# Optimization experiments

Hardware: AMD Instinct MI355X
Metric: run time of the kernel (lower is better)

## Reference

```python
import jax, jax.numpy as jnp
import numpy as np

N = 20000      # nodes
E = 320000     # edges (before self loops)
C = 128        # hidesize (in = out channels)
H = 5          # attention heads
NEG_SLOPE = 0.2
EPS = 1e-16


def setup_inputs() -> dict:
    key = jax.random.key(0)
    k1, k2, k3, k4, k5, k6 = jax.random.split(key, 6)
    features = jax.random.normal(k1, (N, C), dtype=jnp.float32)
    edge_index = jax.random.randint(k2, (2, E), 0, N, dtype=jnp.int64)
    # GATConv parameters: shared linear for src/dst, per-head attention vectors, bias
    W = jax.random.normal(k3, (C, H * C), dtype=jnp.float32) * (1.0 / np.sqrt(C))
    att_src = jax.random.normal(k4, (H, C), dtype=jnp.float32) * 0.1
    att_dst = jax.random.normal(k5, (H, C), dtype=jnp.float32) * 0.1
    bias = jax.random.normal(k6, (C,), dtype=jnp.float32) * 0.1
    return {"features": features, "W": W, "att_src": att_src,
            "att_dst": att_dst, "bias": bias, "edge_index": edge_index}


def _gat_forward(features, W, att_src, att_dst, bias, edge_index):
    n = features.shape[0]
    # add_self_loops=True: append (i -> i) for every node
    loop = jnp.arange(n, dtype=edge_index.dtype)
    src = jnp.concatenate([edge_index[0], loop])  # message source j
    dst = jnp.concatenate([edge_index[1], loop])  # aggregation target i

    h = (features @ W).reshape(n, H, C)           # [N,H,C] projected per head
    alpha_src = jnp.sum(h * att_src, axis=-1)     # [N,H]
    alpha_dst = jnp.sum(h * att_dst, axis=-1)     # [N,H]

    e = alpha_src[src] + alpha_dst[dst]           # [E',H]
    e = jax.nn.leaky_relu(e, negative_slope=NEG_SLOPE)

    # segment softmax over edges grouped by destination node
    e_max = jax.ops.segment_max(e, dst, num_segments=n)   # [N,H]
    e = jnp.exp(e - e_max[dst])
    denom = jax.ops.segment_sum(e, dst, num_segments=n)   # [N,H]
    alpha = e / (denom[dst] + EPS)                         # [E',H]

    msg = h[src] * alpha[:, :, None]                       # [E',H,C]
    out = jax.ops.segment_sum(msg, dst, num_segments=n)    # [N,H,C]
    out = out.mean(axis=1) + bias                          # concat=False -> head mean
    return features + out                                  # use_residual=True


def reference(features, W, att_src, att_dst, bias, edge_index):
    return _gat_forward(features, W, att_src, att_dst, bias, edge_index)
```

## Files before the change

kernel.cpp:

```cpp
#include <hip/hip_runtime.h>
#include <hip/hip_bf16.h>
#include <stdint.h>

#define C_DIM 128
#define H_DIM 5
#define PAD_DEG 64

typedef __bf16 bf16x8 __attribute__((ext_vector_type(8)));
typedef float f32x4 __attribute__((ext_vector_type(4)));
typedef float f32x2 __attribute__((ext_vector_type(2)));

static __device__ __forceinline__ ushort f2bf(float x) {
    __hip_bfloat16 b = __float2bfloat16(x);
    return *reinterpret_cast<ushort*>(&b);
}

__global__ __launch_bounds__(256) void prep0_kernel(
    const float* __restrict__ F, const float* __restrict__ W,
    const float* __restrict__ att_src, const float* __restrict__ att_dst,
    ushort* __restrict__ Abf, ushort* __restrict__ Bt, float* __restrict__ Wa,
    const int* __restrict__ srcArr, const int* __restrict__ dstArr,
    int* __restrict__ cnt, int* __restrict__ colp,
    int Bw, int Bb, int Bc, int N, int E) {
    int b = blockIdx.x;
    int tid = threadIdx.x;
    if (b < Bw) {
        int t = b * 256 + tid;
        if (t < C_DIM * 10) {
            int k = t / 10, j = t % 10;
            int h = j % 5;
            const float* att = ((j < 5) ? att_src : att_dst) + h * C_DIM;
            const float* w = W + (size_t)k * (H_DIM * C_DIM) + h * C_DIM;
            float sum = 0.f;
#pragma unroll 8
            for (int c = 0; c < C_DIM; ++c) sum = fmaf(w[c], att[c], sum);
            Wa[k * 10 + j] = sum;
        }
    } else if (b < Bw + Bb) {
        int t = (b - Bw) * 256 + tid;
        if (t < 640 * 128) {
            int c = t >> 7, k = t & 127;
            Bt[t] = f2bf(W[(size_t)k * 640 + c]);
        }
    } else if (b < Bw + Bb + Bc) {
        int t = (b - Bw - Bb) * 256 + tid;
        if (t < N * 16) {
            const float4* f4 = reinterpret_cast<const float4*>(F) + (size_t)t * 2;
            float4 v0 = f4[0], v1 = f4[1];
            float vv[8] = {v0.x, v0.y, v0.z, v0.w, v1.x, v1.y, v1.z, v1.w};
            ushort u[8];
#pragma unroll
            for (int i = 0; i < 8; ++i) u[i] = f2bf(vv[i]);
            *reinterpret_cast<uint4*>(Abf + (size_t)t * 8) = *reinterpret_cast<uint4*>(u);
        }
    } else {
        int e = (b - Bw - Bb - Bc) * 256 + tid;
        if (e < E + N) {
            int s, i;
            if (e < E) { s = srcArr[e]; i = dstArr[e]; }
            else       { s = e - E;    i = s; }
            int pos = atomicAdd(&cnt[i], 1);
            if (pos < PAD_DEG) colp[(size_t)i * PAD_DEG + pos] = s;
        }
    }
}

__global__ __launch_bounds__(256) void gemm_alpha_kernel(
    const ushort* __restrict__ Abf, const ushort* __restrict__ Bt,
    unsigned char* __restrict__ Hout,
    const float* __restrict__ F, const float* __restrict__ Wa,
    float* __restrict__ asrc, float* __restrict__ adst,
    int NBG, int NRB, int N) {
    __shared__ char smem[52224];
    int tid = threadIdx.x;
    if ((int)blockIdx.x < NBG) {
        ushort (*As)[136] = reinterpret_cast<ushort(*)[136]>(smem);
        ushort (*Bs)[136] = reinterpret_cast<ushort(*)[136]>(smem + 128 * 136 * 2);
        int by = blockIdx.x % NRB;
        int bx = blockIdx.x / NRB;
        int row0 = by * 128, col0 = bx * 64;
        int seg = tid & 15, rb = tid >> 4;
#pragma unroll
        for (int p = 0; p < 8; ++p) {
            int r = rb + p * 16;
            int gr = row0 + r;
            uint4 v = make_uint4(0u, 0u, 0u, 0u);
            if (gr < N) v = *reinterpret_cast<const uint4*>(Abf + (size_t)gr * 128 + seg * 8);
            *reinterpret_cast<uint4*>(&As[r][seg * 8]) = v;
        }
#pragma unroll
        for (int p = 0; p < 4; ++p) {
            int r = rb + p * 16;
            uint4 v = *reinterpret_cast<const uint4*>(Bt + (size_t)(col0 + r) * 128 + seg * 8);
            *reinterpret_cast<uint4*>(&Bs[r][seg * 8]) = v;
        }
        __syncthreads();
        int wave = tid >> 6, lane = tid & 63;
        int wr = (wave & 1) * 64;
        int wc = (wave >> 1) * 32;
        int lm = lane & 15, lk = (lane >> 4) * 8;
        f32x4 acc[4][2] = {};
#pragma unroll
        for (int kk = 0; kk < 4; ++kk) {
            int k = kk * 32 + lk;
            bf16x8 a[4], bvec[2];
#pragma unroll
            for (int m = 0; m < 4; ++m)
                a[m] = *reinterpret_cast<const bf16x8*>(&As[wr + m * 16 + lm][k]);
#pragma unroll
            for (int n = 0; n < 2; ++n)
                bvec[n] = *reinterpret_cast<const bf16x8*>(&Bs[wc + n * 16 + lm][k]);
#pragma unroll
            for (int m = 0; m < 4; ++m)
#pragma unroll
                for (int n = 0; n < 2; ++n)
                    acc[m][n] = __builtin_amdgcn_mfma_f32_16x16x32_bf16(a[m], bvec[n], acc[m][n], 0, 0, 0);
        }
        int r4 = (lane >> 4) * 4;
#pragma unroll
        for (int m = 0; m < 4; ++m) {
#pragma unroll
            for (int r = 0; r < 4; ++r) {
                int grow = row0 + wr + m * 16 + r4 + r;
                if (grow < N) {
                    int pk = __builtin_amdgcn_cvt_pk_fp8_f32(acc[m][0][r], acc[m][1][r], 0, false);
                    unsigned char* rowp = Hout + (size_t)grow * 640 + col0 + wc;
                    rowp[lm]      = (unsigned char)(pk & 0xff);
                    rowp[16 + lm] = (unsigned char)((pk >> 8) & 0xff);
                }
            }
        }
    } else {
        float (*f_lds)[132] = reinterpret_cast<float(*)[132]>(smem);
        float* wa_lds = reinterpret_cast<float*>(smem + 16 * 132 * 4);
        int node0 = ((int)blockIdx.x - NBG) * 16;
#pragma unroll
        for (int t = 0; t < 2; ++t) {
            int idx = tid + t * 256;
            int n = idx >> 5, c4 = idx & 31;
            int node = node0 + n;
            float4 v = make_float4(0.f, 0.f, 0.f, 0.f);
            if (node < N) v = *(reinterpret_cast<const float4*>(F) + (size_t)node * 32 + c4);
            f_lds[n][c4 * 4 + 0] = v.x;
            f_lds[n][c4 * 4 + 1] = v.y;
            f_lds[n][c4 * 4 + 2] = v.z;
            f_lds[n][c4 * 4 + 3] = v.w;
        }
#pragma unroll
        for (int t = 0; t < 5; ++t) {
            int idx = tid + t * 256;
            if (idx < 1280) wa_lds[idx] = Wa[idx];
        }
        __syncthreads();
        if (tid < 160) {
            int n = tid / 10, j = tid % 10;
            int node = node0 + n;
            if (node < N) {
                float sum = 0.f;
#pragma unroll 8
                for (int k = 0; k < C_DIM; ++k) sum = fmaf(f_lds[n][k], wa_lds[k * 10 + j], sum);
                if (j < 5) asrc[node * 5 + j] = sum;
                else       adst[node * 5 + (j - 5)] = sum;
            }
        }
    }
}

__global__ __launch_bounds__(256) void gat_aggregate(
    const int* __restrict__ cnt, const int* __restrict__ colp,
    const float* __restrict__ asrc, const float* __restrict__ adst,
    const unsigned char* __restrict__ h8,
    const float* __restrict__ features, const float* __restrict__ bias,
    float* __restrict__ out, int N) {
    int node = blockIdx.x * 4 + (threadIdx.x >> 6);
    if (node >= N) return;
    int lane = threadIdx.x & 63;
    int g = lane >> 4, m = lane & 15;
    float adg = adst[node * 5 + g];
    float ad4 = adst[node * 5 + 4];
    const int offA = g * 128 + m * 8;
    const int offB = 512 + lane * 2;
    int deg = cnt[node];
    if (deg > PAD_DEG) deg = PAD_DEG;
    const int* cp = colp + (size_t)node * PAD_DEG;
    float accG[8] = {};
    float acc4a = 0.f, acc4b = 0.f;
    float sg = 0.f, s4 = 0.f;
    int p = 0;
    for (; p + 4 <= deg; p += 4) {
        int jj[4];
#pragma unroll
        for (int b = 0; b < 4; ++b) jj[b] = cp[p + b];
        uint2 q[4]; ushort q4[4];
#pragma unroll
        for (int b = 0; b < 4; ++b) {
            const unsigned char* hp = h8 + (size_t)jj[b] * 640;
            q[b]  = *reinterpret_cast<const uint2*>(hp + offA);
            q4[b] = *reinterpret_cast<const ushort*>(hp + offB);
        }
#pragma unroll
        for (int b = 0; b < 4; ++b) {
            float eg = asrc[jj[b] * 5 + g] + adg;
            float e4 = asrc[jj[b] * 5 + 4] + ad4;
            eg = (eg > 0.f) ? eg : 0.2f * eg;
            e4 = (e4 > 0.f) ? e4 : 0.2f * e4;
            float wg = __expf(eg), w4 = __expf(e4);
            sg += wg; s4 += w4;
            f32x2 x01 = __builtin_amdgcn_cvt_pk_f32_fp8((int)q[b].x, false);
            f32x2 x23 = __builtin_amdgcn_cvt_pk_f32_fp8((int)q[b].x, true);
            f32x2 x45 = __builtin_amdgcn_cvt_pk_f32_fp8((int)q[b].y, false);
            f32x2 x67 = __builtin_amdgcn_cvt_pk_f32_fp8((int)q[b].y, true);
            accG[0] = fmaf(wg, x01[0], accG[0]);
            accG[1] = fmaf(wg, x01[1], accG[1]);
            accG[2] = fmaf(wg, x23[0], accG[2]);
            accG[3] = fmaf(wg, x23[1], accG[3]);
            accG[4] = fmaf(wg, x45[0], accG[4]);
            accG[5] = fmaf(wg, x45[1], accG[5]);
            accG[6] = fmaf(wg, x67[0], accG[6]);
            accG[7] = fmaf(wg, x67[1], accG[7]);
            f32x2 y = __builtin_amdgcn_cvt_pk_f32_fp8((int)q4[b], false);
            acc4a = fmaf(w4, y[0], acc4a);
            acc4b = fmaf(w4, y[1], acc4b);
        }
    }
    for (; p < deg; ++p) {
        int j = cp[p];
        float eg = asrc[j * 5 + g] + adg;
        float e4 = asrc[j * 5 + 4] + ad4;
        eg = (eg > 0.f) ? eg : 0.2f * eg;
        e4 = (e4 > 0.f) ? e4 : 0.2f * e4;
        float wg = __expf(eg), w4 = __expf(e4);
        sg += wg; s4 += w4;
        const unsigned char* hp = h8 + (size_t)j * 640;
        uint2 q = *reinterpret_cast<const uint2*>(hp + offA);
        ushort q4 = *reinterpret_cast<const ushort*>(hp + offB);
        f32x2 x01 = __builtin_amdgcn_cvt_pk_f32_fp8((int)q.x, false);
        f32x2 x23 = __builtin_amdgcn_cvt_pk_f32_fp8((int)q.x, true);
        f32x2 x45 = __builtin_amdgcn_cvt_pk_f32_fp8((int)q.y, false);
        f32x2 x67 = __builtin_amdgcn_cvt_pk_f32_fp8((int)q.y, true);
        accG[0] = fmaf(wg, x01[0], accG[0]);
        accG[1] = fmaf(wg, x01[1], accG[1]);
        accG[2] = fmaf(wg, x23[0], accG[2]);
        accG[3] = fmaf(wg, x23[1], accG[3]);
        accG[4] = fmaf(wg, x45[0], accG[4]);
        accG[5] = fmaf(wg, x45[1], accG[5]);
        accG[6] = fmaf(wg, x67[0], accG[6]);
        accG[7] = fmaf(wg, x67[1], accG[7]);
        f32x2 y = __builtin_amdgcn_cvt_pk_f32_fp8((int)q4, false);
        acc4a = fmaf(w4, y[0], acc4a);
        acc4b = fmaf(w4, y[1], acc4b);
    }
    float invg = 1.f / (sg + 1e-16f);
    float r[8];
#pragma unroll
    for (int e = 0; e < 8; ++e) r[e] = accG[e] * invg;
#pragma unroll
    for (int e = 0; e < 8; ++e) r[e] += __shfl_xor(r[e], 16, 64);
#pragma unroll
    for (int e = 0; e < 8; ++e) r[e] += __shfl_xor(r[e], 32, 64);
    float inv4 = 1.f / (s4 + 1e-16f);
#pragma unroll
    for (int i = 0; i < 8; ++i) {
        int srcl = 4 * m + (i >> 1);
        float h4 = __shfl((i & 1) ? acc4b : acc4a, srcl, 64);
        r[i] = fmaf(h4, inv4, r[i]);
    }
    if (g == 0) {
        int c0 = m * 8;
        size_t base = (size_t)node * 128 + c0;
        float4 f0 = *reinterpret_cast<const float4*>(features + base);
        float4 f1 = *reinterpret_cast<const float4*>(features + base + 4);
        float4 b0 = *reinterpret_cast<const float4*>(bias + c0);
        float4 b1 = *reinterpret_cast<const float4*>(bias + c0 + 4);
        float4 o0, o1;
        o0.x = f0.x + b0.x + 0.2f * r[0];
        o0.y = f0.y + b0.y + 0.2f * r[1];
        o0.z = f0.z + b0.z + 0.2f * r[2];
        o0.w = f0.w + b0.w + 0.2f * r[3];
        o1.x = f1.x + b1.x + 0.2f * r[4];
        o1.y = f1.y + b1.y + 0.2f * r[5];
        o1.z = f1.z + b1.z + 0.2f * r[6];
        o1.w = f1.w + b1.w + 0.2f * r[7];
        *reinterpret_cast<float4*>(out + base) = o0;
        *reinterpret_cast<float4*>(out + base + 4) = o1;
    }
}

static inline char* bump(char*& p, size_t bytes) {
    char* r = p;
    p += (bytes + 255) & ~(size_t)255;
    return r;
}

extern "C" void kernel_launch(void* const* d_in, const int* in_sizes, int n_in,
                              void* d_out, int out_size, void* d_ws, size_t ws_size,
                              hipStream_t stream) {
    const float* features = (const float*)d_in[0];
    const float* W        = (const float*)d_in[1];
    const float* att_src  = (const float*)d_in[2];
    const float* att_dst  = (const float*)d_in[3];
    const float* bias     = (const float*)d_in[4];
    const int*   edges    = (const int*)d_in[5];

    const int N = in_sizes[0] / C_DIM;
    const int E = in_sizes[5] / 2;
    const int EN = E + N;
    const int* srcArr = edges;
    const int* dstArr = edges + E;

    char* p = (char*)d_ws;
    float* Wa     = (float*)bump(p, C_DIM * 10 * sizeof(float));
    float* asrc   = (float*)bump(p, (size_t)N * 5 * sizeof(float));
    float* adst   = (float*)bump(p, (size_t)N * 5 * sizeof(float));
    unsigned char* h8 = (unsigned char*)bump(p, (size_t)N * 640);
    ushort* Abf   = (ushort*)bump(p, (size_t)N * C_DIM * sizeof(ushort));
    ushort* Bt    = (ushort*)bump(p, 640 * 128 * sizeof(ushort));
    int* cnt      = (int*)bump(p, (size_t)N * sizeof(int));
    int* colp     = (int*)bump(p, (size_t)N * PAD_DEG * sizeof(int));

    float* out = (float*)d_out;

    hipMemsetAsync(cnt, 0, (size_t)N * sizeof(int), stream);

    const int Bw = (C_DIM * 10 + 255) / 256;
    const int Bb = (640 * 128 + 255) / 256;
    const int Bc = (N * 16 + 255) / 256;
    const int G0 = Bw + Bb + Bc + (EN + 255) / 256;
    prep0_kernel<<<G0, 256, 0, stream>>>(features, W, att_src, att_dst, Abf, Bt, Wa,
                                         srcArr, dstArr, cnt, colp, Bw, Bb, Bc, N, E);
    const int NRB = (N + 127) / 128;
    const int NBG = NRB * 10;
    const int G1 = NBG + (N + 15) / 16;
    gemm_alpha_kernel<<<G1, 256, 0, stream>>>(Abf, Bt, h8, features, Wa, asrc, adst,
                                              NBG, NRB, N);
    gat_aggregate<<<(N + 3) / 4, 256, 0, stream>>>(cnt, colp, asrc, adst, h8, features,
                                                   bias, out, N);
}
```

Measured before the change: 87.45 us.

## Fuse attention-score reduction into per-head GEMM epilogue with atomics

The separate Wa precompute and the alpha blocks (features·Wa) are removed. Attention scores are now computed inside the GEMM epilogue from the fp32 accumulators, reduced across lanes with shuffles and accumulated with atomics. Each GEMM block now covers a full head (two 64-column passes) instead of one 64-column tile, which halves the block count and reuses the A tile across both passes. A custom zero kernel replaces the memset so asrc, adst and cnt are cleared together, and the edge-scatter blocks are placed first in prep0. The cost is atomic traffic and a little less parallelism in the GEMM launch.

New measurement: 101.4 us. +16.0%, slower.

```diff
diff --git a/kernel.cpp b/kernel.cpp
--- a/kernel.cpp
+++ b/kernel.cpp
@@ -15,46 +15,25 @@
     return *reinterpret_cast<ushort*>(&b);
 }
 
+__global__ __launch_bounds__(256) void zero_kernel(int* __restrict__ buf, int total) {
+    int idx = (blockIdx.x * 256 + threadIdx.x) * 4;
+    if (idx + 3 < total) {
+        *reinterpret_cast<int4*>(buf + idx) = make_int4(0, 0, 0, 0);
+    } else {
+        for (int k = idx; k < total; ++k) buf[k] = 0;
+    }
+}
+
 __global__ __launch_bounds__(256) void prep0_kernel(
     const float* __restrict__ F, const float* __restrict__ W,
-    const float* __restrict__ att_src, const float* __restrict__ att_dst,
-    ushort* __restrict__ Abf, ushort* __restrict__ Bt, float* __restrict__ Wa,
+    ushort* __restrict__ Abf, ushort* __restrict__ Bt,
     const int* __restrict__ srcArr, const int* __restrict__ dstArr,
     int* __restrict__ cnt, int* __restrict__ colp,
-    int Bw, int Bb, int Bc, int N, int E) {
+    int Bs_, int Bb, int N, int E) {
     int b = blockIdx.x;
     int tid = threadIdx.x;
-    if (b < Bw) {
-        int t = b * 256 + tid;
-        if (t < C_DIM * 10) {
-            int k = t / 10, j = t % 10;
-            int h = j % 5;
-            const float* att = ((j < 5) ? att_src : att_dst) + h * C_DIM;
-            const float* w = W + (size_t)k * (H_DIM * C_DIM) + h * C_DIM;
-            float sum = 0.f;
-#pragma unroll 8
-            for (int c = 0; c < C_DIM; ++c) sum = fmaf(w[c], att[c], sum);
-            Wa[k * 10 + j] = sum;
-        }
-    } else if (b < Bw + Bb) {
-        int t = (b - Bw) * 256 + tid;
-        if (t < 640 * 128) {
-            int c = t >> 7, k = t & 127;
-            Bt[t] = f2bf(W[(size_t)k * 640 + c]);
-        }
-    } else if (b < Bw + Bb + Bc) {
-        int t = (b - Bw - Bb) * 256 + tid;
-        if (t < N * 16) {
-            const float4* f4 = reinterpret_cast<const float4*>(F) + (size_t)t * 2;
-            float4 v0 = f4[0], v1 = f4[1];
-            float vv[8] = {v0.x, v0.y, v0.z, v0.w, v1.x, v1.y, v1.z, v1.w};
-            ushort u[8];
-#pragma unroll
-            for (int i = 0; i < 8; ++i) u[i] = f2bf(vv[i]);
-            *reinterpret_cast<uint4*>(Abf + (size_t)t * 8) = *reinterpret_cast<uint4*>(u);
-        }
-    } else {
-        int e = (b - Bw - Bb - Bc) * 256 + tid;
+    if (b < Bs_) {
+        int e = b * 256 + tid;
         if (e < E + N) {
             int s, i;
             if (e < E) { s = srcArr[e]; i = dstArr[e]; }
@@ -62,32 +41,56 @@
             int pos = atomicAdd(&cnt[i], 1);
             if (pos < PAD_DEG) colp[(size_t)i * PAD_DEG + pos] = s;
         }
-    }
-}
-
-__global__ __launch_bounds__(256) void gemm_alpha_kernel(
+    } else if (b < Bs_ + Bb) {
+        int t = (b - Bs_) * 256 + tid;
+        if (t < 640 * 128) {
+            int c = t >> 7, k = t & 127;
+            Bt[t] = f2bf(W[(size_t)k * 640 + c]);
+        }
+    } else {
+        int t = (b - Bs_ - Bb) * 256 + tid;
+        if (t < N * 16) {
+            const float4* f4 = reinterpret_cast<const float4*>(F) + (size_t)t * 2;
+            float4 v0 = f4[0], v1 = f4[1];
+            float vv[8] = {v0.x, v0.y, v0.z, v0.w, v1.x, v1.y, v1.z, v1.w};
+            ushort u[8];
+#pragma unroll
+            for (int i = 0; i < 8; ++i) u[i] = f2bf(vv[i]);
+            *reinterpret_cast<uint4*>(Abf + (size_t)t * 8) = *reinterpret_cast<uint4*>(u);
+        }
+    }
+}
+
+__global__ __launch_bounds__(256) void gemm_h_alpha(
     const ushort* __restrict__ Abf, const ushort* __restrict__ Bt,
-    unsigned char* __restrict__ Hout,
-    const float* __restrict__ F, const float* __restrict__ Wa,
-    float* __restrict__ asrc, float* __restrict__ adst,
-    int NBG, int NRB, int N) {
-    __shared__ char smem[52224];
+    const float* __restrict__ att_src, const float* __restrict__ att_dst,
+    unsigned char* __restrict__ Hout, float* __restrict__ asrc, float* __restrict__ adst,
+    int NRB, int N) {
+    __shared__ ushort As[128][136];
+    __shared__ ushort Bs[64][136];
     int tid = threadIdx.x;
-    if ((int)blockIdx.x < NBG) {
-        ushort (*As)[136] = reinterpret_cast<ushort(*)[136]>(smem);
-        ushort (*Bs)[136] = reinterpret_cast<ushort(*)[136]>(smem + 128 * 136 * 2);
-        int by = blockIdx.x % NRB;
-        int bx = blockIdx.x / NRB;
-        int row0 = by * 128, col0 = bx * 64;
-        int seg = tid & 15, rb = tid >> 4;
-#pragma unroll
-        for (int p = 0; p < 8; ++p) {
-            int r = rb + p * 16;
-            int gr = row0 + r;
-            uint4 v = make_uint4(0u, 0u, 0u, 0u);
-            if (gr < N) v = *reinterpret_cast<const uint4*>(Abf + (size_t)gr * 128 + seg * 8);
-            *reinterpret_cast<uint4*>(&As[r][seg * 8]) = v;
-        }
+    int by = blockIdx.x % NRB;
+    int head = blockIdx.x / NRB;
+    int row0 = by * 128;
+    int seg = tid & 15, rb = tid >> 4;
+#pragma unroll
+    for (int p = 0; p < 8; ++p) {
+        int r = rb + p * 16;
+        int gr = row0 + r;
+        uint4 v = make_uint4(0u, 0u, 0u, 0u);
+        if (gr < N) v = *reinterpret_cast<const uint4*>(Abf + (size_t)gr * 128 + seg * 8);
+        *reinterpret_cast<uint4*>(&As[r][seg * 8]) = v;
+    }
+    int wave = tid >> 6, lane = tid & 63;
+    int wr = (wave & 1) * 64;
+    int wc = (wave >> 1) * 32;
+    int lm = lane & 15, lk = (lane >> 4) * 8;
+    int r4 = (lane >> 4) * 4;
+    float alps[4][4] = {};
+    float alpd[4][4] = {};
+    for (int cb = 0; cb < 2; ++cb) {
+        int col0 = head * 128 + cb * 64;
+        if (cb) __syncthreads();
 #pragma unroll
         for (int p = 0; p < 4; ++p) {
             int r = rb + p * 16;
@@ -95,10 +98,6 @@
             *reinterpret_cast<uint4*>(&Bs[r][seg * 8]) = v;
         }
         __syncthreads();
-        int wave = tid >> 6, lane = tid & 63;
-        int wr = (wave & 1) * 64;
-        int wc = (wave >> 1) * 32;
-        int lm = lane & 15, lk = (lane >> 4) * 8;
         f32x4 acc[4][2] = {};
 #pragma unroll
         for (int kk = 0; kk < 4; ++kk) {
@@ -116,7 +115,13 @@
                 for (int n = 0; n < 2; ++n)
                     acc[m][n] = __builtin_amdgcn_mfma_f32_16x16x32_bf16(a[m], bvec[n], acc[m][n], 0, 0, 0);
         }
-        int r4 = (lane >> 4) * 4;
+        float asv[2], adv[2];
+#pragma unroll
+        for (int n = 0; n < 2; ++n) {
+            int cw = cb * 64 + wc + n * 16 + lm;
+            asv[n] = att_src[head * C_DIM + cw];
+            adv[n] = att_dst[head * C_DIM + cw];
+        }
 #pragma unroll
         for (int m = 0; m < 4; ++m) {
 #pragma unroll
@@ -128,39 +133,31 @@
                     rowp[lm]      = (unsigned char)(pk & 0xff);
                     rowp[16 + lm] = (unsigned char)((pk >> 8) & 0xff);
                 }
+                alps[m][r] = fmaf(acc[m][0][r], asv[0], fmaf(acc[m][1][r], asv[1], alps[m][r]));
+                alpd[m][r] = fmaf(acc[m][0][r], adv[0], fmaf(acc[m][1][r], adv[1], alpd[m][r]));
             }
         }
-    } else {
-        float (*f_lds)[132] = reinterpret_cast<float(*)[132]>(smem);
-        float* wa_lds = reinterpret_cast<float*>(smem + 16 * 132 * 4);
-        int node0 = ((int)blockIdx.x - NBG) * 16;
-#pragma unroll
-        for (int t = 0; t < 2; ++t) {
-            int idx = tid + t * 256;
-            int n = idx >> 5, c4 = idx & 31;
-            int node = node0 + n;
-            float4 v = make_float4(0.f, 0.f, 0.f, 0.f);
-            if (node < N) v = *(reinterpret_cast<const float4*>(F) + (size_t)node * 32 + c4);
-            f_lds[n][c4 * 4 + 0] = v.x;
-            f_lds[n][c4 * 4 + 1] = v.y;
-            f_lds[n][c4 * 4 + 2] = v.z;
-            f_lds[n][c4 * 4 + 3] = v.w;
-        }
-#pragma unroll
-        for (int t = 0; t < 5; ++t) {
-            int idx = tid + t * 256;
-            if (idx < 1280) wa_lds[idx] = Wa[idx];
-        }
-        __syncthreads();
-        if (tid < 160) {
-            int n = tid / 10, j = tid % 10;
-            int node = node0 + n;
-            if (node < N) {
-                float sum = 0.f;
-#pragma unroll 8
-                for (int k = 0; k < C_DIM; ++k) sum = fmaf(f_lds[n][k], wa_lds[k * 10 + j], sum);
-                if (j < 5) asrc[node * 5 + j] = sum;
-                else       adst[node * 5 + (j - 5)] = sum;
+    }
+#pragma unroll
+    for (int m = 0; m < 4; ++m) {
+#pragma unroll
+        for (int r = 0; r < 4; ++r) {
+            float v = alps[m][r];
+            v += __shfl_xor(v, 1, 64);
+            v += __shfl_xor(v, 2, 64);
+            v += __shfl_xor(v, 4, 64);
+            v += __shfl_xor(v, 8, 64);
+            float w = alpd[m][r];
+            w += __shfl_xor(w, 1, 64);
+            w += __shfl_xor(w, 2, 64);
+            w += __shfl_xor(w, 4, 64);
+            w += __shfl_xor(w, 8, 64);
+            if (lm == 0) {
+                int grow = row0 + wr + m * 16 + r4 + r;
+                if (grow < N) {
+                    atomicAdd(&asrc[grow * 5 + head], v);
+                    atomicAdd(&adst[grow * 5 + head], w);
+                }
             }
         }
     }
@@ -309,30 +306,27 @@
     const int* dstArr = edges + E;
 
     char* p = (char*)d_ws;
-    float* Wa     = (float*)bump(p, C_DIM * 10 * sizeof(float));
-    float* asrc   = (float*)bump(p, (size_t)N * 5 * sizeof(float));
-    float* adst   = (float*)bump(p, (size_t)N * 5 * sizeof(float));
+    float* zbuf   = (float*)bump(p, (size_t)11 * N * sizeof(float));
+    float* asrc   = zbuf;
+    float* adst   = zbuf + (size_t)5 * N;
+    int*   cnt    = (int*)(zbuf + (size_t)10 * N);
     unsigned char* h8 = (unsigned char*)bump(p, (size_t)N * 640);
     ushort* Abf   = (ushort*)bump(p, (size_t)N * C_DIM * sizeof(ushort));
     ushort* Bt    = (ushort*)bump(p, 640 * 128 * sizeof(ushort));
-    int* cnt      = (int*)bump(p, (size_t)N * sizeof(int));
     int* colp     = (int*)bump(p, (size_t)N * PAD_DEG * sizeof(int));
 
     float* out = (float*)d_out;
 
-    hipMemsetAsync(cnt, 0, (size_t)N * sizeof(int), stream);
-
-    const int Bw = (C_DIM * 10 + 255) / 256;
+    const int ztotal = 11 * N;
+    zero_kernel<<<(ztotal / 4 + 255) / 256, 256, 0, stream>>>((int*)zbuf, ztotal);
+    const int Bs_ = (EN + 255) / 256;
     const int Bb = (640 * 128 + 255) / 256;
     const int Bc = (N * 16 + 255) / 256;
-    const int G0 = Bw + Bb + Bc + (EN + 255) / 256;
-    prep0_kernel<<<G0, 256, 0, stream>>>(features, W, att_src, att_dst, Abf, Bt, Wa,
-                                         srcArr, dstArr, cnt, colp, Bw, Bb, Bc, N, E);
+    prep0_kernel<<<Bs_ + Bb + Bc, 256, 0, stream>>>(features, W, Abf, Bt,
+                                                    srcArr, dstArr, cnt, colp, Bs_, Bb, N, E);
     const int NRB = (N + 127) / 128;
-    const int NBG = NRB * 10;
-    const int G1 = NBG + (N + 15) / 16;
-    gemm_alpha_kernel<<<G1, 256, 0, stream>>>(Abf, Bt, h8, features, Wa, asrc, adst,
-                                              NBG, NRB, N);
+    gemm_h_alpha<<<NRB * 5, 256, 0, stream>>>(Abf, Bt, att_src, att_dst, h8, asrc, adst,
+                                              NRB, N);
     gat_aggregate<<<(N + 3) / 4, 256, 0, stream>>>(cnt, colp, asrc, adst, h8, features,
                                                    bias, out, N);
 }
```
